# Kernel tuning notes

Measured on AMD Instinct MI355X. Metric: run time of the kernel, lower is better.

The kernel has to match this reference:

```python
import jax, jax.numpy as jnp
import numpy as np

B, F, S, H1, O = 8192, 128, 128, 64, 1

def setup_inputs() -> dict:
    key = jax.random.key(0)
    ks = jax.random.split(key, 8)
    sc1 = 1.0  # Linear(1, S): torch init ~ U(-1,1); use scaled normals
    return {
        "x":  jax.random.normal(ks[0], (B, F), dtype=jnp.float32),
        "W1": jax.random.normal(ks[1], (F, S), dtype=jnp.float32) * sc1,
        "b1": jax.random.normal(ks[2], (F, S), dtype=jnp.float32) * 0.1,
        "W2": jax.random.normal(ks[3], (F, S, H1), dtype=jnp.float32) * (1.0 / np.sqrt(S)),
        "b2": jax.random.normal(ks[4], (F, H1), dtype=jnp.float32) * 0.1,
        "W3": jax.random.normal(ks[5], (F, H1, O), dtype=jnp.float32) * (1.0 / np.sqrt(H1)),
        "b3": jax.random.normal(ks[6], (F, O), dtype=jnp.float32) * 0.1,
        "bias": jnp.zeros((O,), dtype=jnp.float32),
    }

def reference(x, W1, b1, W2, b2, W3, b3, bias):
    # Per-feature net: Linear(1,S) -> ReLU -> Linear(S,H1) -> ReLU -> (Dropout=id at eval) -> Linear(H1,O)
    # Batched over the feature axis f (equivalent to the original Python loop + cat).
    h1 = jax.nn.relu(x[:, :, None] * W1[None, :, :] + b1[None, :, :])      # [B,F,S]
    h2 = jax.nn.relu(jnp.einsum('bfs,fsh->bfh', h1, W2) + b2[None, :, :])  # [B,F,H1]
    fo = jnp.einsum('bfh,fho->bfo', h2, W3) + b3[None, :, :]               # [B,F,O]
    # torch.cat(...,dim=1) of [B,1] slices -> [B,F]; sum(dim=1,keepdim=True)+bias -> [B,1]
    out = fo.reshape(B, F * O).sum(axis=1, keepdims=True) + bias           # [B,1]
    return out
```

## Files before the change

### kernel.cpp

```cpp
#include <hip/hip_runtime.h>
#include <hip/hip_bf16.h>

#define B_ 8192
#define F_ 128
#define S_ 128
#define H_ 64

typedef __attribute__((ext_vector_type(4))) float f32x4;
typedef __attribute__((ext_vector_type(8))) short bf16x8;

__global__ __launch_bounds__(256) void nam_init(float* __restrict__ out,
                                                const float* __restrict__ bias) {
    int i = blockIdx.x * 256 + threadIdx.x;
    if (i < B_) out[i] = bias[0];
}

static __device__ __forceinline__ short f2bf(float v) {
    __hip_bfloat16 t = __float2bfloat16(v);
    return __builtin_bit_cast(short, t);
}

__global__ __launch_bounds__(256) void nam_prep(const float* __restrict__ W2,
                                                bf16x8* __restrict__ W2bf) {
    const int idx = blockIdx.x * 256 + threadIdx.x;
    const int l   = idx & 63;
    const int m   = (idx >> 6) & 3;
    const int kk  = (idx >> 8) & 3;
    const int f   = idx >> 10;
    const int l16 = l & 15, lg = l >> 4;

    const float* __restrict__ src =
        W2 + ((size_t)f * S_ + kk * 32 + lg * 8) * H_ + m * 16 + l16;
    bf16x8 v;
#pragma unroll
    for (int j = 0; j < 8; ++j) v[j] = f2bf(src[j * H_]);
    W2bf[idx] = v;
}

__global__ __launch_bounds__(256) void nam_xt(const float* __restrict__ x,
                                              float* __restrict__ xT) {
    __shared__ float t[32][33];
    const int li = threadIdx.x & 31;
    const int wi = threadIdx.x >> 5;
    const int b0 = (blockIdx.x & 255) * 32;
    const int f0 = (blockIdx.x >> 8) * 32;
#pragma unroll
    for (int r = wi; r < 32; r += 8)
        t[r][li] = x[(size_t)(b0 + r) * F_ + f0 + li];
    __syncthreads();
#pragma unroll
    for (int r = wi; r < 32; r += 8)
        xT[(size_t)(f0 + r) * B_ + b0 + li] = t[li][r];
}

__global__ __launch_bounds__(256, 4) void nam_mfma(
    const float* __restrict__ x,
    const float* __restrict__ xT,
    const float* __restrict__ W1,
    const float* __restrict__ b1,
    const bf16x8* __restrict__ W2bf,
    const float* __restrict__ b2,
    const float* __restrict__ W3,
    const float* __restrict__ b3,
    float* __restrict__ out)
{
    const int f   = blockIdx.x >> 6;
    const int bt  = blockIdx.x & 63;
    const int tid = threadIdx.x;
    const int w   = tid >> 6;
    const int l   = tid & 63;
    const int l16 = l & 15;
    const int lg  = l >> 4;

    const int bbase = bt * 128 + w * 32;

    const float* __restrict__ W1f = W1 + f * S_;
    const float* __restrict__ b1f = b1 + f * S_;
    const bf16x8* __restrict__ W2f = W2bf + (size_t)f * 16 * 64 + l;

    float xv0, xv1;
    if (xT) {
        xv0 = xT[(size_t)f * B_ + bbase + l16];
        xv1 = xT[(size_t)f * B_ + bbase + 16 + l16];
    } else {
        xv0 = x[(size_t)(bbase + l16) * F_ + f];
        xv1 = x[(size_t)(bbase + 16 + l16) * F_ + f];
    }

    f32x4 acc[4][2];
#pragma unroll
    for (int m = 0; m < 4; ++m) {
        acc[m][0] = (f32x4){0.f, 0.f, 0.f, 0.f};
        acc[m][1] = (f32x4){0.f, 0.f, 0.f, 0.f};
    }

#pragma unroll 1
    for (int kk = 0; kk < 4; ++kk) {
        bf16x8 afrag[4];
#pragma unroll
        for (int m = 0; m < 4; ++m)
            afrag[m] = W2f[(kk * 4 + m) * 64];

        const int s0 = kk * 32 + lg * 8;
        const f32x4 w1a = *(const f32x4*)(W1f + s0);
        const f32x4 w1b = *(const f32x4*)(W1f + s0 + 4);
        const f32x4 b1a = *(const f32x4*)(b1f + s0);
        const f32x4 b1b = *(const f32x4*)(b1f + s0 + 4);

        bf16x8 bf0, bf1;
#pragma unroll
        for (int j = 0; j < 4; ++j) {
            bf0[j]     = f2bf(fmaxf(fmaf(xv0, w1a[j], b1a[j]), 0.f));
            bf0[j + 4] = f2bf(fmaxf(fmaf(xv0, w1b[j], b1b[j]), 0.f));
            bf1[j]     = f2bf(fmaxf(fmaf(xv1, w1a[j], b1a[j]), 0.f));
            bf1[j + 4] = f2bf(fmaxf(fmaf(xv1, w1b[j], b1b[j]), 0.f));
        }

#pragma unroll
        for (int m = 0; m < 4; ++m) {
            acc[m][0] = __builtin_amdgcn_mfma_f32_16x16x32_bf16(afrag[m], bf0, acc[m][0], 0, 0, 0);
            acc[m][1] = __builtin_amdgcn_mfma_f32_16x16x32_bf16(afrag[m], bf1, acc[m][1], 0, 0, 0);
        }
    }

    const float* __restrict__ b2f = b2 + f * H_;
    const float* __restrict__ W3f = W3 + f * H_;
    const float b3f = b3[f];

    float fo0 = 0.f, fo1 = 0.f;
#pragma unroll
    for (int m = 0; m < 4; ++m) {
        const f32x4 b2v = *(const f32x4*)(b2f + m * 16 + lg * 4);
        const f32x4 w3v = *(const f32x4*)(W3f + m * 16 + lg * 4);
#pragma unroll
        for (int r = 0; r < 4; ++r) {
            fo0 = fmaf(fmaxf(acc[m][0][r] + b2v[r], 0.f), w3v[r], fo0);
            fo1 = fmaf(fmaxf(acc[m][1][r] + b2v[r], 0.f), w3v[r], fo1);
        }
    }
    fo0 += __shfl_xor(fo0, 16);
    fo0 += __shfl_xor(fo0, 32);
    fo1 += __shfl_xor(fo1, 16);
    fo1 += __shfl_xor(fo1, 32);
    if (lg == 0) {
        atomicAdd(&out[bbase + l16], fo0 + b3f);
        atomicAdd(&out[bbase + 16 + l16], fo1 + b3f);
    }
}

extern "C" void kernel_launch(void* const* d_in, const int* in_sizes, int n_in,
                              void* d_out, int out_size, void* d_ws, size_t ws_size,
                              hipStream_t stream) {
    const float* x    = (const float*)d_in[0];
    const float* W1   = (const float*)d_in[1];
    const float* b1   = (const float*)d_in[2];
    const float* W2   = (const float*)d_in[3];
    const float* b2   = (const float*)d_in[4];
    const float* W3   = (const float*)d_in[5];
    const float* b3   = (const float*)d_in[6];
    const float* bias = (const float*)d_in[7];
    float* out = (float*)d_out;

    bf16x8* W2bf = (bf16x8*)d_ws;
    const size_t W2BF_BYTES = (size_t)F_ * 16 * 64 * 16;
    const size_t XT_BYTES   = (size_t)F_ * B_ * 4;
    float* xT = (ws_size >= W2BF_BYTES + XT_BYTES)
                    ? (float*)((char*)d_ws + W2BF_BYTES) : nullptr;

    nam_init<<<(B_ + 255) / 256, 256, 0, stream>>>(out, bias);
    nam_prep<<<(F_ * 16 * 64) / 256, 256, 0, stream>>>(W2, W2bf);
    if (xT)
        nam_xt<<<(B_ / 32) * (F_ / 32), 256, 0, stream>>>(x, xT);
    nam_mfma<<<F_ * (B_ / 128), 256, 0, stream>>>(x, xT, W1, b1, W2bf, b2, W3, b3, out);
}
```

Before: 119.6 us.

## Merge prologue kernels and make MFMA blocks persistent per feature chunk

The three setup kernels (output init, W2 bf16 repack, x transpose) become one prologue launch that branches on block index, removing two launch gaps. The main kernel now runs 8 blocks per feature instead of 64. Each wave loads all 16 W2 fragments plus W1/b1/b2/W3 once into registers and loops over 8 batch tiles, prefetching the next x values, so per-feature weights are no longer reloaded for every small tile. In exchange, register pressure rises (launch bounds drop to 2 blocks/SM), the grid shrinks to 1024 blocks, and the non-transposed fallback when the workspace is too small is gone.

```diff
diff --git a/kernel.cpp b/kernel.cpp
--- a/kernel.cpp
+++ b/kernel.cpp
@@ -5,56 +5,56 @@
 #define F_ 128
 #define S_ 128
 #define H_ 64
+#define NCHUNK 8
 
 typedef __attribute__((ext_vector_type(4))) float f32x4;
 typedef __attribute__((ext_vector_type(8))) short bf16x8;
-
-__global__ __launch_bounds__(256) void nam_init(float* __restrict__ out,
-                                                const float* __restrict__ bias) {
-    int i = blockIdx.x * 256 + threadIdx.x;
-    if (i < B_) out[i] = bias[0];
-}
 
 static __device__ __forceinline__ short f2bf(float v) {
     __hip_bfloat16 t = __float2bfloat16(v);
     return __builtin_bit_cast(short, t);
 }
 
-__global__ __launch_bounds__(256) void nam_prep(const float* __restrict__ W2,
-                                                bf16x8* __restrict__ W2bf) {
-    const int idx = blockIdx.x * 256 + threadIdx.x;
-    const int l   = idx & 63;
-    const int m   = (idx >> 6) & 3;
-    const int kk  = (idx >> 8) & 3;
-    const int f   = idx >> 10;
-    const int l16 = l & 15, lg = l >> 4;
-
-    const float* __restrict__ src =
-        W2 + ((size_t)f * S_ + kk * 32 + lg * 8) * H_ + m * 16 + l16;
-    bf16x8 v;
+__global__ __launch_bounds__(256) void nam_prologue(
+    const float* __restrict__ bias, float* __restrict__ out,
+    const float* __restrict__ W2,   bf16x8* __restrict__ W2bf,
+    const float* __restrict__ x,    float* __restrict__ xT)
+{
+    __shared__ float t[32][33];
+    const int blk = blockIdx.x;
+    if (blk < 32) {
+        int i = blk * 256 + threadIdx.x;
+        out[i] = bias[0];
+    } else if (blk < 544) {
+        const int idx = (blk - 32) * 256 + threadIdx.x;
+        const int l   = idx & 63;
+        const int m   = (idx >> 6) & 3;
+        const int kk  = (idx >> 8) & 3;
+        const int f   = idx >> 10;
+        const int l16 = l & 15, lg = l >> 4;
+        const float* __restrict__ src =
+            W2 + ((size_t)f * S_ + kk * 32 + lg * 8) * H_ + m * 16 + l16;
+        bf16x8 v;
 #pragma unroll
-    for (int j = 0; j < 8; ++j) v[j] = f2bf(src[j * H_]);
-    W2bf[idx] = v;
+        for (int j = 0; j < 8; ++j) v[j] = f2bf(src[j * H_]);
+        W2bf[idx] = v;
+    } else {
+        const int bid = blk - 544;
+        const int li = threadIdx.x & 31;
+        const int wi = threadIdx.x >> 5;
+        const int b0 = (bid & 255) * 32;
+        const int f0 = (bid >> 8) * 32;
+#pragma unroll
+        for (int r = wi; r < 32; r += 8)
+            t[r][li] = x[(size_t)(b0 + r) * F_ + f0 + li];
+        __syncthreads();
+#pragma unroll
+        for (int r = wi; r < 32; r += 8)
+            xT[(size_t)(f0 + r) * B_ + b0 + li] = t[li][r];
+    }
 }
 
-__global__ __launch_bounds__(256) void nam_xt(const float* __restrict__ x,
-                                              float* __restrict__ xT) {
-    __shared__ float t[32][33];
-    const int li = threadIdx.x & 31;
-    const int wi = threadIdx.x >> 5;
-    const int b0 = (blockIdx.x & 255) * 32;
-    const int f0 = (blockIdx.x >> 8) * 32;
-#pragma unroll
-    for (int r = wi; r < 32; r += 8)
-        t[r][li] = x[(size_t)(b0 + r) * F_ + f0 + li];
-    __syncthreads();
-#pragma unroll
-    for (int r = wi; r < 32; r += 8)
-        xT[(size_t)(f0 + r) * B_ + b0 + li] = t[li][r];
-}
-
-__global__ __launch_bounds__(256, 4) void nam_mfma(
-    const float* __restrict__ x,
+__global__ __launch_bounds__(256, 2) void nam_mfma(
     const float* __restrict__ xT,
     const float* __restrict__ W1,
     const float* __restrict__ b1,
@@ -64,87 +64,98 @@
     const float* __restrict__ b3,
     float* __restrict__ out)
 {
-    const int f   = blockIdx.x >> 6;
-    const int bt  = blockIdx.x & 63;
-    const int tid = threadIdx.x;
-    const int w   = tid >> 6;
-    const int l   = tid & 63;
-    const int l16 = l & 15;
-    const int lg  = l >> 4;
+    const int f     = blockIdx.x >> 3;
+    const int chunk = blockIdx.x & 7;
+    const int tid   = threadIdx.x;
+    const int w     = tid >> 6;
+    const int l     = tid & 63;
+    const int l16   = l & 15;
+    const int lg    = l >> 4;
 
-    const int bbase = bt * 128 + w * 32;
+    const int b0 = chunk * (B_ / NCHUNK) + w * 256;
+
+    const bf16x8* __restrict__ W2f = W2bf + (size_t)f * 16 * 64 + l;
+    bf16x8 afrag[16];
+#pragma unroll
+    for (int q = 0; q < 16; ++q) afrag[q] = W2f[q * 64];
 
     const float* __restrict__ W1f = W1 + f * S_;
     const float* __restrict__ b1f = b1 + f * S_;
-    const bf16x8* __restrict__ W2f = W2bf + (size_t)f * 16 * 64 + l;
-
-    float xv0, xv1;
-    if (xT) {
-        xv0 = xT[(size_t)f * B_ + bbase + l16];
-        xv1 = xT[(size_t)f * B_ + bbase + 16 + l16];
-    } else {
-        xv0 = x[(size_t)(bbase + l16) * F_ + f];
-        xv1 = x[(size_t)(bbase + 16 + l16) * F_ + f];
-    }
-
-    f32x4 acc[4][2];
+    f32x4 w1r[8], b1r[8];
 #pragma unroll
-    for (int m = 0; m < 4; ++m) {
-        acc[m][0] = (f32x4){0.f, 0.f, 0.f, 0.f};
-        acc[m][1] = (f32x4){0.f, 0.f, 0.f, 0.f};
-    }
-
-#pragma unroll 1
     for (int kk = 0; kk < 4; ++kk) {
-        bf16x8 afrag[4];
-#pragma unroll
-        for (int m = 0; m < 4; ++m)
-            afrag[m] = W2f[(kk * 4 + m) * 64];
-
-        const int s0 = kk * 32 + lg * 8;
-        const f32x4 w1a = *(const f32x4*)(W1f + s0);
-        const f32x4 w1b = *(const f32x4*)(W1f + s0 + 4);
-        const f32x4 b1a = *(const f32x4*)(b1f + s0);
-        const f32x4 b1b = *(const f32x4*)(b1f + s0 + 4);
-
-        bf16x8 bf0, bf1;
-#pragma unroll
-        for (int j = 0; j < 4; ++j) {
-            bf0[j]     = f2bf(fmaxf(fmaf(xv0, w1a[j], b1a[j]), 0.f));
-            bf0[j + 4] = f2bf(fmaxf(fmaf(xv0, w1b[j], b1b[j]), 0.f));
-            bf1[j]     = f2bf(fmaxf(fmaf(xv1, w1a[j], b1a[j]), 0.f));
-            bf1[j + 4] = f2bf(fmaxf(fmaf(xv1, w1b[j], b1b[j]), 0.f));
-        }
-
-#pragma unroll
-        for (int m = 0; m < 4; ++m) {
-            acc[m][0] = __builtin_amdgcn_mfma_f32_16x16x32_bf16(afrag[m], bf0, acc[m][0], 0, 0, 0);
-            acc[m][1] = __builtin_amdgcn_mfma_f32_16x16x32_bf16(afrag[m], bf1, acc[m][1], 0, 0, 0);
-        }
+        w1r[kk * 2]     = *(const f32x4*)(W1f + kk * 32 + lg * 8);
+        w1r[kk * 2 + 1] = *(const f32x4*)(W1f + kk * 32 + lg * 8 + 4);
+        b1r[kk * 2]     = *(const f32x4*)(b1f + kk * 32 + lg * 8);
+        b1r[kk * 2 + 1] = *(const f32x4*)(b1f + kk * 32 + lg * 8 + 4);
     }
 
     const float* __restrict__ b2f = b2 + f * H_;
     const float* __restrict__ W3f = W3 + f * H_;
-    const float b3f = b3[f];
-
-    float fo0 = 0.f, fo1 = 0.f;
+    f32x4 b2v[4], w3v[4];
 #pragma unroll
     for (int m = 0; m < 4; ++m) {
-        const f32x4 b2v = *(const f32x4*)(b2f + m * 16 + lg * 4);
-        const f32x4 w3v = *(const f32x4*)(W3f + m * 16 + lg * 4);
+        b2v[m] = *(const f32x4*)(b2f + m * 16 + lg * 4);
+        w3v[m] = *(const f32x4*)(W3f + m * 16 + lg * 4);
+    }
+    const float b3f = b3[f];
+    const float* __restrict__ xTf = xT + (size_t)f * B_;
+
+    float xv0 = xTf[b0 + l16];
+    float xv1 = xTf[b0 + 16 + l16];
+
+#pragma unroll 1
+    for (int it = 0; it < 8; ++it) {
+        const int bbase = b0 + it * 32;
+        float nx0 = 0.f, nx1 = 0.f;
+        if (it < 7) {
+            nx0 = xTf[bbase + 32 + l16];
+            nx1 = xTf[bbase + 48 + l16];
+        }
+
+        f32x4 acc[4][2];
 #pragma unroll
-        for (int r = 0; r < 4; ++r) {
-            fo0 = fmaf(fmaxf(acc[m][0][r] + b2v[r], 0.f), w3v[r], fo0);
-            fo1 = fmaf(fmaxf(acc[m][1][r] + b2v[r], 0.f), w3v[r], fo1);
+        for (int m = 0; m < 4; ++m) {
+            acc[m][0] = (f32x4){0.f, 0.f, 0.f, 0.f};
+            acc[m][1] = (f32x4){0.f, 0.f, 0.f, 0.f};
         }
-    }
-    fo0 += __shfl_xor(fo0, 16);
-    fo0 += __shfl_xor(fo0, 32);
-    fo1 += __shfl_xor(fo1, 16);
-    fo1 += __shfl_xor(fo1, 32);
-    if (lg == 0) {
-        atomicAdd(&out[bbase + l16], fo0 + b3f);
-        atomicAdd(&out[bbase + 16 + l16], fo1 + b3f);
+
+#pragma unroll
+        for (int kk = 0; kk < 4; ++kk) {
+            bf16x8 bf0, bf1;
+#pragma unroll
+            for (int j = 0; j < 4; ++j) {
+                bf0[j]     = f2bf(fmaxf(fmaf(xv0, w1r[kk*2][j],     b1r[kk*2][j]),     0.f));
+                bf0[j + 4] = f2bf(fmaxf(fmaf(xv0, w1r[kk*2+1][j],   b1r[kk*2+1][j]),   0.f));
+                bf1[j]     = f2bf(fmaxf(fmaf(xv1, w1r[kk*2][j],     b1r[kk*2][j]),     0.f));
+                bf1[j + 4] = f2bf(fmaxf(fmaf(xv1, w1r[kk*2+1][j],   b1r[kk*2+1][j]),   0.f));
+            }
+#pragma unroll
+            for (int m = 0; m < 4; ++m) {
+                acc[m][0] = __builtin_amdgcn_mfma_f32_16x16x32_bf16(afrag[kk*4+m], bf0, acc[m][0], 0, 0, 0);
+                acc[m][1] = __builtin_amdgcn_mfma_f32_16x16x32_bf16(afrag[kk*4+m], bf1, acc[m][1], 0, 0, 0);
+            }
+        }
+
+        float fo0 = 0.f, fo1 = 0.f;
+#pragma unroll
+        for (int m = 0; m < 4; ++m) {
+#pragma unroll
+            for (int r = 0; r < 4; ++r) {
+                fo0 = fmaf(fmaxf(acc[m][0][r] + b2v[m][r], 0.f), w3v[m][r], fo0);
+                fo1 = fmaf(fmaxf(acc[m][1][r] + b2v[m][r], 0.f), w3v[m][r], fo1);
+            }
+        }
+        fo0 += __shfl_xor(fo0, 16);
+        fo0 += __shfl_xor(fo0, 32);
+        fo1 += __shfl_xor(fo1, 16);
+        fo1 += __shfl_xor(fo1, 32);
+        if (lg == 0) {
+            atomicAdd(&out[bbase + l16], fo0 + b3f);
+            atomicAdd(&out[bbase + 16 + l16], fo1 + b3f);
+        }
+        xv0 = nx0;
+        xv1 = nx1;
     }
 }
 
@@ -163,13 +174,8 @@
 
     bf16x8* W2bf = (bf16x8*)d_ws;
     const size_t W2BF_BYTES = (size_t)F_ * 16 * 64 * 16;
-    const size_t XT_BYTES   = (size_t)F_ * B_ * 4;
-    float* xT = (ws_size >= W2BF_BYTES + XT_BYTES)
-                    ? (float*)((char*)d_ws + W2BF_BYTES) : nullptr;
+    float* xT = (float*)((char*)d_ws + W2BF_BYTES);
 
-    nam_init<<<(B_ + 255) / 256, 256, 0, stream>>>(out, bias);
-    nam_prep<<<(F_ * 16 * 64) / 256, 256, 0, stream>>>(W2, W2bf);
-    if (xT)
-        nam_xt<<<(B_ / 32) * (F_ / 32), 256, 0, stream>>>(x, xT);
-    nam_mfma<<<F_ * (B_ / 128), 256, 0, stream>>>(x, xT, W1, b1, W2bf, b2, W3, b3, out);
+    nam_prologue<<<32 + 512 + 1024, 256, 0, stream>>>(bias, out, W2, W2bf, x, xT);
+    nam_mfma<<<F_ * NCHUNK, 256, 0, stream>>>(xT, W1, b1, W2bf, b2, W3, b3, out);
 }
```

Measured after the change: 96.61 us. 19.2% less time.
